# Kernel tuning notes

Hardware: AMD Instinct MI355X
Metric: run time of the kernel (lower is better)

## Reference

```python
import jax, jax.numpy as jnp
import numpy as np

L = 4096
E = 512   # embed dim
S = 1024  # state dim
H = 150   # Scorer hidden dim
GI = 2 * S + E
MAX_N = 10


def _scorer(x, W1, b1, W2, b2, W3, b3):
    h = jax.nn.relu(x @ W1 + b1)
    h = jax.nn.relu(h @ W2 + b2)
    return h @ W3 + b3  # [..., 1]


def setup_inputs() -> dict:
    key = jax.random.key(0)
    ks = jax.random.split(key, 16)
    def init(k, shape, fan_in):
        return jax.random.normal(k, shape, dtype=jnp.float32) / np.sqrt(fan_in)
    inp = {
        "embeds": jax.random.normal(ks[0], (L, E), dtype=jnp.float32),
        "states": jax.random.normal(ks[1], (L, S), dtype=jnp.float32),
        # attention Scorer params (input S)
        "aW1": init(ks[2], (S, H), S), "ab1": jnp.zeros((H,), jnp.float32),
        "aW2": init(ks[3], (H, H), H), "ab2": jnp.zeros((H,), jnp.float32),
        "aW3": init(ks[4], (H, 1), H), "ab3": jnp.zeros((1,), jnp.float32),
        # sm Scorer params (input GI)
        "sW1": init(ks[5], (GI, H), GI), "sb1": jnp.zeros((H,), jnp.float32),
        "sW2": init(ks[6], (H, H), H), "sb2": jnp.zeros((H,), jnp.float32),
        "sW3": init(ks[7], (H, 1), H), "sb3": jnp.zeros((1,), jnp.float32),
    }
    return inp


def reference(embeds, states, aW1, ab1, aW2, ab2, aW3, ab3,
              sW1, sb1, sW2, sb2, sW3, sb3):
    # per-token attention logits, computed once: [L]
    attns = _scorer(states, aW1, ab1, aW2, ab2, aW3, ab3)[:, 0]

    gs = []
    for n in range(1, MAX_N + 1):  # fixed small loop over window sizes
        M = L - n + 1                                  # number of windows
        starts = jnp.arange(M)
        idx = starts[:, None] + jnp.arange(n)          # [M, n] token indices
        w = jax.nn.softmax(attns[idx], axis=1)         # windowed softmax [M, n]
        pooled = jnp.einsum('mn,mne->me', w, embeds[idx])  # [M, E]
        g = jnp.concatenate([states[starts], states[starts + n - 1], pooled],
                            axis=1)                    # [M, 2S+E]
        gs.append(g)
    x = jnp.concatenate(gs, axis=0)                    # [T, GI], T = 10L-45
    scores = _scorer(x, sW1, sb1, sW2, sb2, sW3, sb3)[:, 0]  # [T]
    return scores
```

## Files before the change

### kernel.cpp

```cpp
#include <hip/hip_runtime.h>
#include <math.h>

#define LTOK 4096
#define EDIM 512
#define SDIM 1024
#define HDIM 150
#define SEG 160
#define MAXN 10
#define TOTAL_ROWS 40915
#define KA 1536
#define NKT 48
#define K2 160
#define NCG 42

typedef _Float16 hfrag __attribute__((ext_vector_type(8)));
typedef _Float16 h4 __attribute__((ext_vector_type(4)));
typedef float ffrag __attribute__((ext_vector_type(4)));


#define ITEMS_A   (LTOK * (KA / 8))
#define ITEMS_W   (NCG * NKT * 64)
#define ITEMS_W2  (K2 * (K2 / 8))
#define ITEMS_A2  (K2 * (K2 / 8))
#define ITEMS_TOT (ITEMS_A + ITEMS_W + ITEMS_W2 + ITEMS_A2)

__global__ __launch_bounds__(256) void prep_kernel(
    const float* __restrict__ embeds, const float* __restrict__ states,
    const float* __restrict__ aW1, const float* __restrict__ aW2,
    const float* __restrict__ sW1, const float* __restrict__ sW2,
    _Float16* __restrict__ Apk, _Float16* __restrict__ Wpk,
    _Float16* __restrict__ W2pk, _Float16* __restrict__ A2pk)
{
    int it = blockIdx.x * 256 + threadIdx.x;
    if (it < ITEMS_A) {
        const int rem = it % (NKT * 64);
        const int g = it / (NKT * 64), kt = rem >> 6, lane = rem & 63;
        const int row = g * 16 + (lane & 15);
        const int k0 = kt * 32 + (lane >> 4) * 8;
        const float* src = (k0 < SDIM) ? (states + (size_t)row * SDIM + k0)
                                       : (embeds + (size_t)row * EDIM + (k0 - SDIM));
        const float4 v0 = *(const float4*)src;
        const float4 v1 = *(const float4*)(src + 4);
        _Float16 o[8] = {(_Float16)v0.x, (_Float16)v0.y, (_Float16)v0.z, (_Float16)v0.w,
                         (_Float16)v1.x, (_Float16)v1.y, (_Float16)v1.z, (_Float16)v1.w};
        *(uint4*)(Apk + (size_t)it * 8) = *(uint4*)o;
        return;
    }
    it -= ITEMS_A;
    if (it < ITEMS_W) {
        const int rem = it % (NKT * 64);
        const int cgi = it / (NKT * 64), kt = rem >> 6, lane = rem & 63;
        const int col = cgi * 16 + (lane & 15);
        const int k0 = kt * 32 + (lane >> 4) * 8;
        _Float16 o[8];
        for (int j = 0; j < 8; ++j) {
            const int k = k0 + j;
            float wv = 0.f;
            if (col < 160) {
                if (col < HDIM && k < SDIM) wv = sW1[(size_t)k * HDIM + col];
            } else if (col < 320) {
                const int cj = col - 160;
                if (cj < HDIM && k < SDIM) wv = sW1[(size_t)(SDIM + k) * HDIM + cj];
            } else if (col < 480) {
                const int cj = col - 320;
                if (cj < HDIM && k >= SDIM) wv = sW1[(size_t)(SDIM + k) * HDIM + cj];
            } else if (col >= 512) {
                const int cj = col - 512;
                if (cj < HDIM && k < SDIM) wv = aW1[(size_t)k * HDIM + cj];
            }
            o[j] = (_Float16)wv;
        }
        *(uint4*)(Wpk + ((size_t)((size_t)cgi * NKT + kt) * 64 + lane) * 8) = *(uint4*)o;
        return;
    }
    it -= ITEMS_W;
    if (it < ITEMS_W2 + ITEMS_A2) {
        const bool is_a = (it >= ITEMS_W2);
        const int li = is_a ? (it - ITEMS_W2) : it;
        const float* src = is_a ? aW2 : sW2;
        _Float16* dst = is_a ? A2pk : W2pk;
        const int tk = li >> 6, lane = li & 63;
        const int col = (tk / 5) * 16 + (lane & 15);
        const int k0 = (tk % 5) * 32 + (lane >> 4) * 8;
        _Float16 o[8];
        for (int j = 0; j < 8; ++j) {
            const int k = k0 + j;
            float wv = (col < HDIM && k < HDIM) ? src[(size_t)k * HDIM + col] : 0.f;
            o[j] = (_Float16)wv;
        }
        *(uint4*)(dst + ((size_t)tk * 64 + lane) * 8) = *(uint4*)o;
    }
}

__global__ __launch_bounds__(256) void k_proj(
    const _Float16* __restrict__ Apk, const _Float16* __restrict__ Wpk,
    const _Float16* __restrict__ A2pk,
    const float* __restrict__ ab1, const float* __restrict__ ab2,
    const float* __restrict__ aW3, const float* __restrict__ ab3,
    _Float16* __restrict__ P1h, _Float16* __restrict__ P2h,
    _Float16* __restrict__ PEh, float* __restrict__ attns)
{
    const int bid = blockIdx.x;
    const int tid = threadIdx.x;
    const int w = tid >> 6, lane = tid & 63;
    const int quad = lane >> 4, l16 = lane & 15;

    __shared__ __align__(16) _Float16 ah1[64 * SEG];

    if (bid < 64) {
        const int tok0 = bid * 64;
        const int g = tok0 / 16 + w;

        ffrag acc[10];
#pragma unroll
        for (int c = 0; c < 10; ++c) acc[c] = (ffrag){0.f, 0.f, 0.f, 0.f};

        const _Float16* ap = Apk + ((size_t)g * NKT) * 512 + lane * 8;
        for (int kt = 0; kt < 32; ++kt) {
            const hfrag a = *(const hfrag*)(ap + (size_t)kt * 512);
#pragma unroll
            for (int c = 0; c < 10; ++c) {
                const hfrag b = *(const hfrag*)(
                    Wpk + (((size_t)(32 + c) * NKT + kt) * 64 + lane) * 8);
                acc[c] = __builtin_amdgcn_mfma_f32_16x16x32_f16(a, b, acc[c], 0, 0, 0);
            }
        }
#pragma unroll
        for (int c = 0; c < 10; ++c) {
            const int col = c * 16 + l16;
            const float b1 = (col < HDIM) ? ab1[col] : 0.f;
#pragma unroll
            for (int r = 0; r < 4; ++r) {
                const int row = w * 16 + quad * 4 + r;
                ah1[row * SEG + col] = (_Float16)fmaxf(acc[c][r] + b1, 0.f);
            }
        }
        __syncthreads();

        hfrag af[5];
#pragma unroll
        for (int ks = 0; ks < 5; ++ks)
            af[ks] = *(const hfrag*)&ah1[(w * 16 + l16) * SEG + ks * 32 + quad * 8];

        float part[4] = {0.f, 0.f, 0.f, 0.f};
        for (int ct = 0; ct < 10; ++ct) {
            ffrag a2 = (ffrag){0.f, 0.f, 0.f, 0.f};
#pragma unroll
            for (int ks = 0; ks < 5; ++ks) {
                const hfrag fb = *(const hfrag*)(
                    A2pk + ((size_t)(ct * 5 + ks) * 64 + lane) * 8);
                a2 = __builtin_amdgcn_mfma_f32_16x16x32_f16(af[ks], fb, a2, 0, 0, 0);
            }
            const int col = ct * 16 + l16;
            const float s2 = (col < HDIM) ? ab2[col] : 0.f;
            const float s3 = (col < HDIM) ? aW3[col] : 0.f;
#pragma unroll
            for (int r = 0; r < 4; ++r) part[r] += fmaxf(a2[r] + s2, 0.f) * s3;
        }
#pragma unroll
        for (int off = 1; off < 16; off <<= 1) {
#pragma unroll
            for (int r = 0; r < 4; ++r) part[r] += __shfl_xor(part[r], off, 64);
        }
        if (l16 == 0) {
            const float b3 = ab3[0];
#pragma unroll
            for (int r = 0; r < 4; ++r)
                attns[tok0 + w * 16 + quad * 4 + r] = part[r] + b3;
        }
        return;
    }

    const int tile = bid - 64;
    const int bM = tile & 63, bN = tile >> 6;
    const int wm = w & 1, wn = w >> 1;
    const int gbase = bM * 4 + wm * 2;
    const int cgbase = bN * 4 + wn * 2;
    const int kt0 = (bN >= 5) ? 32 : 0;
    const int kt1 = (bN >= 5) ? 48 : 32;

    ffrag acc[2][2];
#pragma unroll
    for (int t = 0; t < 2; ++t)
#pragma unroll
        for (int u = 0; u < 2; ++u) acc[t][u] = (ffrag){0.f, 0.f, 0.f, 0.f};

    const _Float16* a0p = Apk + ((size_t)(gbase + 0) * NKT) * 512 + lane * 8;
    const _Float16* a1p = Apk + ((size_t)(gbase + 1) * NKT) * 512 + lane * 8;
    const _Float16* b0p = Wpk + ((size_t)(cgbase + 0) * NKT) * 512 + lane * 8;
    const _Float16* b1p = Wpk + ((size_t)(cgbase + 1) * NKT) * 512 + lane * 8;

#pragma unroll 4
    for (int kt = kt0; kt < kt1; ++kt) {
        const hfrag a0 = *(const hfrag*)(a0p + (size_t)kt * 512);
        const hfrag a1 = *(const hfrag*)(a1p + (size_t)kt * 512);
        const hfrag b0 = *(const hfrag*)(b0p + (size_t)kt * 512);
        const hfrag b1 = *(const hfrag*)(b1p + (size_t)kt * 512);
        acc[0][0] = __builtin_amdgcn_mfma_f32_16x16x32_f16(a0, b0, acc[0][0], 0, 0, 0);
        acc[1][0] = __builtin_amdgcn_mfma_f32_16x16x32_f16(a1, b0, acc[1][0], 0, 0, 0);
        acc[0][1] = __builtin_amdgcn_mfma_f32_16x16x32_f16(a0, b1, acc[0][1], 0, 0, 0);
        acc[1][1] = __builtin_amdgcn_mfma_f32_16x16x32_f16(a1, b1, acc[1][1], 0, 0, 0);
    }

#pragma unroll
    for (int t = 0; t < 2; ++t)
#pragma unroll
        for (int u = 0; u < 2; ++u) {
            const int col = (cgbase + u) * 16 + l16;
#pragma unroll
            for (int r = 0; r < 4; ++r) {
                const int row = (gbase + t) * 16 + quad * 4 + r;
                const _Float16 hv = (_Float16)acc[t][u][r];
                if (col < 160)      P1h[(size_t)row * SEG + col] = hv;
                else if (col < 320) P2h[(size_t)row * SEG + (col - 160)] = hv;
                else if (col < 480) PEh[(size_t)row * SEG + (col - 320)] = hv;
            }
        }
}

#define RB2 64
__global__ __launch_bounds__(256) void span_kernel(
    const float* __restrict__ attns, const _Float16* __restrict__ P1h,
    const _Float16* __restrict__ P2h, const _Float16* __restrict__ PEh,
    const float* __restrict__ sb1, const _Float16* __restrict__ W2pk,
    const float* __restrict__ sb2, const float* __restrict__ sW3,
    const float* __restrict__ sb3, float* __restrict__ out)
{
    const int nIdx = blockIdx.x >> 6, mChunk = blockIdx.x & 63;
    const int n = nIdx + 1;
    const int Mn = LTOK - n + 1;
    const int m0 = mChunk * 64;
    const int nrows = min(64, Mn - m0);
    const int offn = nIdx * LTOK - (nIdx * (nIdx - 1)) / 2;

    const int tid = threadIdx.x;
    const int w = tid >> 6, lane = tid & 63, quad = lane >> 4, l16 = lane & 15;

    __shared__ __align__(16) _Float16 h1h[RB2 * K2];
    __shared__ float wgt[RB2][MAXN];

    if (tid < RB2) {
        const int m = min(m0 + tid, Mn - 1);
        float mx = -1e30f;
        for (int j = 0; j < n; ++j) mx = fmaxf(mx, attns[m + j]);
        float tp[MAXN]; float s = 0.f;
        for (int j = 0; j < n; ++j) { tp[j] = expf(attns[m + j] - mx); s += tp[j]; }
        const float inv = 1.f / s;
#pragma unroll
        for (int j = 0; j < MAXN; ++j) wgt[tid][j] = (j < n) ? tp[j] * inv : 0.f;
    }
    __syncthreads();

    for (int item = tid; item < RB2 * (K2 / 4); item += 256) {
        const int r = item / (K2 / 4), cq = item % (K2 / 4);
        const int c0 = cq * 4;
        const int m = min(m0 + r, Mn - 1);
        float4 a = {0.f, 0.f, 0.f, 0.f};
        if (c0 < HDIM) {
            const h4 p1 = *(const h4*)(P1h + (size_t)m * SEG + c0);
            const h4 p2 = *(const h4*)(P2h + (size_t)(m + n - 1) * SEG + c0);
            a.x = (float)p1[0] + (float)p2[0];
            a.y = (float)p1[1] + (float)p2[1];
            a.z = (float)p1[2] + (float)p2[2];
            a.w = (float)p1[3] + (float)p2[3];
#pragma unroll
            for (int j = 0; j < MAXN; ++j) {
                const int mj = min(m + j, LTOK - 1);
                const h4 pe = *(const h4*)(PEh + (size_t)mj * SEG + c0);
                const float wj = wgt[r][j];
                a.x = fmaf(wj, (float)pe[0], a.x);
                a.y = fmaf(wj, (float)pe[1], a.y);
                a.z = fmaf(wj, (float)pe[2], a.z);
                a.w = fmaf(wj, (float)pe[3], a.w);
            }
        }
        _Float16 o[4];
        o[0] = (c0 + 0 < HDIM) ? (_Float16)fmaxf(a.x + sb1[c0 + 0], 0.f) : (_Float16)0.f;
        o[1] = (c0 + 1 < HDIM) ? (_Float16)fmaxf(a.y + sb1[c0 + 1], 0.f) : (_Float16)0.f;
        o[2] = (c0 + 2 < HDIM) ? (_Float16)fmaxf(a.z + sb1[c0 + 2], 0.f) : (_Float16)0.f;
        o[3] = (c0 + 3 < HDIM) ? (_Float16)fmaxf(a.w + sb1[c0 + 3], 0.f) : (_Float16)0.f;
        *(uint2*)&h1h[r * K2 + c0] = *(uint2*)o;
    }
    __syncthreads();

    hfrag af[5];
#pragma unroll
    for (int ks = 0; ks < 5; ++ks)
        af[ks] = *(const hfrag*)&h1h[(w * 16 + l16) * K2 + ks * 32 + quad * 8];

    float part[4] = {0.f, 0.f, 0.f, 0.f};
    for (int ct = 0; ct < 10; ++ct) {
        ffrag acc = (ffrag){0.f, 0.f, 0.f, 0.f};
#pragma unroll
        for (int ks = 0; ks < 5; ++ks) {
            const hfrag fb = *(const hfrag*)(
                W2pk + ((size_t)(ct * 5 + ks) * 64 + lane) * 8);
            acc = __builtin_amdgcn_mfma_f32_16x16x32_f16(af[ks], fb, acc, 0, 0, 0);
        }
        const int col = ct * 16 + l16;
        const float s2 = (col < HDIM) ? sb2[col] : 0.f;
        const float s3 = (col < HDIM) ? sW3[col] : 0.f;
#pragma unroll
        for (int r = 0; r < 4; ++r) part[r] += fmaxf(acc[r] + s2, 0.f) * s3;
    }

#pragma unroll
    for (int off = 1; off < 16; off <<= 1) {
#pragma unroll
        for (int r = 0; r < 4; ++r) part[r] += __shfl_xor(part[r], off, 64);
    }
    if (l16 == 0) {
        const float b3 = sb3[0];
#pragma unroll
        for (int r = 0; r < 4; ++r) {
            const int lr = w * 16 + quad * 4 + r;
            if (lr < nrows) out[offn + m0 + lr] = part[r] + b3;
        }
    }
}

extern "C" void kernel_launch(void* const* d_in, const int* in_sizes, int n_in,
                              void* d_out, int out_size, void* d_ws, size_t ws_size,
                              hipStream_t stream) {
    const float* embeds = (const float*)d_in[0];
    const float* states = (const float*)d_in[1];
    const float* aW1 = (const float*)d_in[2];
    const float* ab1 = (const float*)d_in[3];
    const float* aW2 = (const float*)d_in[4];
    const float* ab2 = (const float*)d_in[5];
    const float* aW3 = (const float*)d_in[6];
    const float* ab3 = (const float*)d_in[7];
    const float* sW1 = (const float*)d_in[8];
    const float* sb1 = (const float*)d_in[9];
    const float* sW2 = (const float*)d_in[10];
    const float* sb2 = (const float*)d_in[11];
    const float* sW3 = (const float*)d_in[12];
    const float* sb3 = (const float*)d_in[13];
    float* out = (float*)d_out;

    float* attns = (float*)d_ws;
    _Float16* P1h  = (_Float16*)(attns + LTOK);
    _Float16* P2h  = P1h + (size_t)LTOK * SEG;
    _Float16* PEh  = P2h + (size_t)LTOK * SEG;
    _Float16* Apk  = PEh + (size_t)LTOK * SEG;
    _Float16* Wpk  = Apk + (size_t)ITEMS_A * 8;
    _Float16* W2pk = Wpk + (size_t)ITEMS_W * 8;
    _Float16* A2pk = W2pk + (size_t)ITEMS_W2 * 8;

    prep_kernel<<<ITEMS_TOT / 256, 256, 0, stream>>>(
        embeds, states, aW1, aW2, sW1, sW2, Apk, Wpk, W2pk, A2pk);
    k_proj<<<576, 256, 0, stream>>>(
        Apk, Wpk, A2pk, ab1, ab2, aW3, ab3, P1h, P2h, PEh, attns);
    span_kernel<<<640, 256, 0, stream>>>(
        attns, P1h, P2h, PEh, sb1, W2pk, sb2, sW3, sb3, out);
}
```

Baseline: 155.9 us.

## Pair adjacent window sizes per block to share P1/PE loads in span kernel

The span kernel now has each block handle two consecutive window sizes (n and n+1) over 32 start positions. The P1 and windowed PE loads, and the bias, are shared between the two sizes, and loads are widened to 8 halves. This aims to cut redundant global reads of the first-layer projections. Separately, the GEMM tiles whose column groups lie beyond the used outputs now exit early to skip wasted MFMA work. The cost is more registers per thread for two accumulator sets, and a smaller M chunk that may reduce reuse of the W2 fragments.

```diff
diff --git a/kernel.cpp b/kernel.cpp
--- a/kernel.cpp
+++ b/kernel.cpp
@@ -14,7 +14,6 @@
 #define NCG 42
 
 typedef _Float16 hfrag __attribute__((ext_vector_type(8)));
-typedef _Float16 h4 __attribute__((ext_vector_type(4)));
 typedef float ffrag __attribute__((ext_vector_type(4)));
 
 
@@ -176,6 +175,7 @@
     const int wm = w & 1, wn = w >> 1;
     const int gbase = bM * 4 + wm * 2;
     const int cgbase = bN * 4 + wn * 2;
+    if (cgbase >= 30) return;
     const int kt0 = (bN >= 5) ? 32 : 0;
     const int kt1 = (bN >= 5) ? 48 : 32;
 
@@ -218,7 +218,6 @@
         }
 }
 
-#define RB2 64
 __global__ __launch_bounds__(256) void span_kernel(
     const float* __restrict__ attns, const _Float16* __restrict__ P1h,
     const _Float16* __restrict__ P2h, const _Float16* __restrict__ PEh,
@@ -226,67 +225,90 @@
     const float* __restrict__ sb2, const float* __restrict__ sW3,
     const float* __restrict__ sb3, float* __restrict__ out)
 {
-    const int nIdx = blockIdx.x >> 6, mChunk = blockIdx.x & 63;
-    const int n = nIdx + 1;
-    const int Mn = LTOK - n + 1;
-    const int m0 = mChunk * 64;
-    const int nrows = min(64, Mn - m0);
-    const int offn = nIdx * LTOK - (nIdx * (nIdx - 1)) / 2;
+    const int pairI = blockIdx.x >> 7;
+    const int mChunk = blockIdx.x & 127;
+    const int n0 = 2 * pairI + 1, n1 = n0 + 1;
+    const int Mn0 = LTOK - n0 + 1, Mn1 = Mn0 - 1;
+    const int m0 = mChunk * 32;
+    const int offn0 = (n0 - 1) * LTOK - ((n0 - 1) * (n0 - 2)) / 2;
+    const int offn1 = offn0 + Mn0;
 
     const int tid = threadIdx.x;
     const int w = tid >> 6, lane = tid & 63, quad = lane >> 4, l16 = lane & 15;
 
-    __shared__ __align__(16) _Float16 h1h[RB2 * K2];
-    __shared__ float wgt[RB2][MAXN];
-
-    if (tid < RB2) {
-        const int m = min(m0 + tid, Mn - 1);
-        float mx = -1e30f;
-        for (int j = 0; j < n; ++j) mx = fmaxf(mx, attns[m + j]);
-        float tp[MAXN]; float s = 0.f;
-        for (int j = 0; j < n; ++j) { tp[j] = expf(attns[m + j] - mx); s += tp[j]; }
-        const float inv = 1.f / s;
-#pragma unroll
-        for (int j = 0; j < MAXN; ++j) wgt[tid][j] = (j < n) ? tp[j] * inv : 0.f;
+    __shared__ __align__(16) _Float16 h1h[2][32 * K2];
+    __shared__ float wgt[2][32][MAXN];
+
+    if (tid < 64) {
+        const int q = tid >> 5, r = tid & 31;
+        const int n = q ? n1 : n0;
+        const int Mn = q ? Mn1 : Mn0;
+        const int m = m0 + r;
+        if (m < Mn) {
+            float mx = -1e30f;
+            for (int j = 0; j < n; ++j) mx = fmaxf(mx, attns[m + j]);
+            float tp[MAXN]; float s = 0.f;
+            for (int j = 0; j < n; ++j) { tp[j] = expf(attns[m + j] - mx); s += tp[j]; }
+            const float inv = 1.f / s;
+#pragma unroll
+            for (int j = 0; j < MAXN; ++j) wgt[q][r][j] = (j < n) ? tp[j] * inv : 0.f;
+        } else {
+#pragma unroll
+            for (int j = 0; j < MAXN; ++j) wgt[q][r][j] = 0.f;
+        }
     }
     __syncthreads();
 
-    for (int item = tid; item < RB2 * (K2 / 4); item += 256) {
-        const int r = item / (K2 / 4), cq = item % (K2 / 4);
-        const int c0 = cq * 4;
-        const int m = min(m0 + r, Mn - 1);
-        float4 a = {0.f, 0.f, 0.f, 0.f};
-        if (c0 < HDIM) {
-            const h4 p1 = *(const h4*)(P1h + (size_t)m * SEG + c0);
-            const h4 p2 = *(const h4*)(P2h + (size_t)(m + n - 1) * SEG + c0);
-            a.x = (float)p1[0] + (float)p2[0];
-            a.y = (float)p1[1] + (float)p2[1];
-            a.z = (float)p1[2] + (float)p2[2];
-            a.w = (float)p1[3] + (float)p2[3];
-#pragma unroll
-            for (int j = 0; j < MAXN; ++j) {
-                const int mj = min(m + j, LTOK - 1);
-                const h4 pe = *(const h4*)(PEh + (size_t)mj * SEG + c0);
-                const float wj = wgt[r][j];
-                a.x = fmaf(wj, (float)pe[0], a.x);
-                a.y = fmaf(wj, (float)pe[1], a.y);
-                a.z = fmaf(wj, (float)pe[2], a.z);
-                a.w = fmaf(wj, (float)pe[3], a.w);
-            }
-        }
-        _Float16 o[4];
-        o[0] = (c0 + 0 < HDIM) ? (_Float16)fmaxf(a.x + sb1[c0 + 0], 0.f) : (_Float16)0.f;
-        o[1] = (c0 + 1 < HDIM) ? (_Float16)fmaxf(a.y + sb1[c0 + 1], 0.f) : (_Float16)0.f;
-        o[2] = (c0 + 2 < HDIM) ? (_Float16)fmaxf(a.z + sb1[c0 + 2], 0.f) : (_Float16)0.f;
-        o[3] = (c0 + 3 < HDIM) ? (_Float16)fmaxf(a.w + sb1[c0 + 3], 0.f) : (_Float16)0.f;
-        *(uint2*)&h1h[r * K2 + c0] = *(uint2*)o;
+    for (int item = tid; item < 32 * (K2 / 8); item += 256) {
+        const int r = item / (K2 / 8), cc = item % (K2 / 8);
+        const int c0 = cc * 8;
+        const int mm = m0 + r;
+        const hfrag p1  = *(const hfrag*)(P1h + (size_t)mm * SEG + c0);
+        const hfrag p2a = *(const hfrag*)(P2h + (size_t)min(mm + n0 - 1, LTOK - 1) * SEG + c0);
+        const hfrag p2b = *(const hfrag*)(P2h + (size_t)min(mm + n0, LTOK - 1) * SEG + c0);
+        float b1v[8];
+#pragma unroll
+        for (int e = 0; e < 8; ++e)
+            b1v[e] = (c0 + e < HDIM) ? sb1[c0 + e] : 0.f;
+        float a0[8], a1[8];
+#pragma unroll
+        for (int e = 0; e < 8; ++e) {
+            a0[e] = (float)p1[e] + (float)p2a[e] + b1v[e];
+            a1[e] = (float)p1[e] + (float)p2b[e] + b1v[e];
+        }
+#pragma unroll
+        for (int j = 0; j < MAXN; ++j) {
+            const int mj = min(mm + j, LTOK - 1);
+            const hfrag pe = *(const hfrag*)(PEh + (size_t)mj * SEG + c0);
+            const float w0j = wgt[0][r][j];
+            const float w1j = wgt[1][r][j];
+#pragma unroll
+            for (int e = 0; e < 8; ++e) {
+                const float pv = (float)pe[e];
+                a0[e] = fmaf(w0j, pv, a0[e]);
+                a1[e] = fmaf(w1j, pv, a1[e]);
+            }
+        }
+        _Float16 o0[8], o1[8];
+#pragma unroll
+        for (int e = 0; e < 8; ++e) {
+            const bool live = (c0 + e < HDIM);
+            o0[e] = live ? (_Float16)fmaxf(a0[e], 0.f) : (_Float16)0.f;
+            o1[e] = live ? (_Float16)fmaxf(a1[e], 0.f) : (_Float16)0.f;
+        }
+        *(uint4*)&h1h[0][r * K2 + c0] = *(uint4*)o0;
+        *(uint4*)&h1h[1][r * K2 + c0] = *(uint4*)o1;
     }
     __syncthreads();
 
+    const int q = w >> 1, rg = w & 1;
+    const int Mq = q ? Mn1 : Mn0;
+    const int offq = q ? offn1 : offn0;
+
     hfrag af[5];
 #pragma unroll
     for (int ks = 0; ks < 5; ++ks)
-        af[ks] = *(const hfrag*)&h1h[(w * 16 + l16) * K2 + ks * 32 + quad * 8];
+        af[ks] = *(const hfrag*)&h1h[q][(rg * 16 + l16) * K2 + ks * 32 + quad * 8];
 
     float part[4] = {0.f, 0.f, 0.f, 0.f};
     for (int ct = 0; ct < 10; ++ct) {
@@ -313,8 +335,8 @@
         const float b3 = sb3[0];
 #pragma unroll
         for (int r = 0; r < 4; ++r) {
-            const int lr = w * 16 + quad * 4 + r;
-            if (lr < nrows) out[offn + m0 + lr] = part[r] + b3;
+            const int lr = rg * 16 + quad * 4 + r;
+            if (m0 + lr < Mq) out[offq + m0 + lr] = part[r] + b3;
         }
     }
 }
```

Measured after the change: 148.8 us. 4.5% less time.
